# Kernel tuning notes

Hardware: AMD Instinct MI355X
Metric: run time of the kernel (lower is better)

## Reference

```python
import jax, jax.numpy as jnp
import numpy as np
import math

NUM_BUCKETS = 32
MAX_DISTANCE = 128
N_HEADS = 16
D_KV = 64
ATTN_SCALE = True


def _relative_position_bucket(relative_position, num_buckets=NUM_BUCKETS, max_distance=MAX_DISTANCE):
    # bidirectional (encoder) variant
    nb = num_buckets // 2
    buckets = (relative_position > 0).astype(jnp.int32) * nb
    rp = jnp.abs(relative_position)
    max_exact = nb // 2
    is_small = rp < max_exact
    rp_large = max_exact + (
        jnp.log(rp.astype(jnp.float32) / max_exact)
        / math.log(max_distance / max_exact)
        * (nb - max_exact)
    ).astype(jnp.int32)
    rp_large = jnp.minimum(rp_large, nb - 1)
    buckets = buckets + jnp.where(is_small, rp, rp_large)
    return buckets


def compute_bias(rel_bias_emb, q_len, k_len):
    ctx = jnp.arange(q_len)[:, None]
    mem = jnp.arange(k_len)[None, :]
    bucket = _relative_position_bucket(mem - ctx)  # [q,k] int32 in [0,32)
    values = rel_bias_emb[bucket]                  # [q,k,H]
    return jnp.transpose(values, (2, 0, 1))[None]  # [1,H,q,k]


def setup_inputs() -> dict:
    key = jax.random.key(0)
    k1, k2, k3, k4 = jax.random.split(key, 4)
    B, S, D = 2, 2048, 1024
    return {
        "hidden_states": jax.random.normal(k1, (B, S, D), jnp.float32),
        "attention_mask": jnp.ones((B, 1, S, S), jnp.float32),
        "W_qkv": jax.random.normal(k2, (D, 3 * D), jnp.float32) * 0.02,
        "W_o": jax.random.normal(k3, (D, D), jnp.float32) * 0.02,
        "rel_bias_emb": jax.random.normal(k4, (NUM_BUCKETS, N_HEADS), jnp.float32) * 0.02,
    }


def reference(hidden_states, attention_mask, W_qkv, W_o, rel_bias_emb):
    B, S, D = hidden_states.shape
    # fused QKV projection (no bias), then split as in split_tensor_along_last_dim
    qkv = jnp.einsum("bsd,de->bse", hidden_states, W_qkv)
    q, k, v = jnp.split(qkv, 3, axis=-1)
    # [b,s,H*d] -> [b,H,s,d]
    def to_heads(t):
        return jnp.transpose(t.reshape(B, S, N_HEADS, D_KV), (0, 2, 1, 3))
    q, k, v = to_heads(q), to_heads(k), to_heads(v)
    scores = jnp.einsum("bhqd,bhkd->bhqk", q, k)
    if ATTN_SCALE:
        scores = scores / math.sqrt(D_KV)
    position_bias = compute_bias(rel_bias_emb, S, S)  # [1,H,S,S]
    scores = scores * attention_mask + (-10000.0 * (1.0 - attention_mask) + position_bias)
    probs = jax.nn.softmax(scores, axis=-1)  # dropout = eval mode (identity)
    ctx = jnp.einsum("bhqk,bhkd->bhqd", probs, v)
    ctx = jnp.transpose(ctx, (0, 2, 1, 3)).reshape(B, S, N_HEADS * D_KV)
    attn_output = jnp.einsum("bse,ed->bsd", ctx, W_o)
    return attn_output
```

## Files before the change

kernel.cpp:

```cpp
#include <hip/hip_runtime.h>
#include <cstdint>

#define DEV static __device__ __forceinline__

typedef __bf16 bf16x8 __attribute__((ext_vector_type(8)));
typedef __bf16 bf16x4 __attribute__((ext_vector_type(4)));
typedef short  s16x4  __attribute__((ext_vector_type(4)));
typedef float  f32x4  __attribute__((ext_vector_type(4)));

DEV unsigned short f32_bf16(float f) {
  union { float f; unsigned u; } v; v.f = f;
  unsigned r = v.u + 0x7FFFu + ((v.u >> 16) & 1u);
  return (unsigned short)(r >> 16);
}

DEV void gload16(const void* g, void* lds) {
  __builtin_amdgcn_global_load_lds((__attribute__((address_space(1))) void*)g,
                                   (__attribute__((address_space(3))) void*)lds,
                                   16, 0, 0);
}

DEV float bcast_lane(float v, int srclane) {
  union { float f; int i; } u; u.f = v;
  u.i = __builtin_amdgcn_ds_bpermute(srclane << 2, u.i);
  return u.f;
}

DEV f32x4 mfma16_bf16(bf16x4 a, bf16x4 b, f32x4 c) {
  union { bf16x4 h; s16x4 s; } ua, ub; ua.h = a; ub.h = b;
#if __has_builtin(__builtin_amdgcn_mfma_f32_16x16x16bf16_1k)
  return __builtin_amdgcn_mfma_f32_16x16x16bf16_1k(ua.s, ub.s, c, 0, 0, 0);
#else
  f32x4 d;
  asm("v_mfma_f32_16x16x16_bf16 %0, %1, %2, %3" : "=v"(d) : "v"(ua.s), "v"(ub.s), "v"(c));
  return d;
#endif
}

__global__ void cast_bf16(const float* __restrict__ x, unsigned short* __restrict__ y) {
  int i = blockIdx.x * 256 + threadIdx.x;
  float4 v = ((const float4*)x)[i];
  uint2 o;
  o.x = (unsigned)f32_bf16(v.x) | ((unsigned)f32_bf16(v.y) << 16);
  o.y = (unsigned)f32_bf16(v.z) | ((unsigned)f32_bf16(v.w) << 16);
  ((uint2*)y)[i] = o;
}

__global__ void transpose_cast(const float* __restrict__ W, unsigned short* __restrict__ WT,
                               int K, int N) {
  __shared__ float t[64][65];
  int k0 = blockIdx.x * 64, n0 = blockIdx.y * 64;
  int tn = threadIdx.x & 63, tk = threadIdx.x >> 6;
#pragma unroll
  for (int i = 0; i < 64; i += 4)
    t[tk + i][tn] = W[(size_t)(k0 + tk + i) * N + n0 + tn];
  __syncthreads();
  int k2 = (threadIdx.x & 31) * 2, n = threadIdx.x >> 5;
#pragma unroll
  for (int i = 0; i < 64; i += 8) {
    int nn = n + i;
    unsigned o = (unsigned)f32_bf16(t[k2][nn]) | ((unsigned)f32_bf16(t[k2 + 1][nn]) << 16);
    *(unsigned*)&WT[(size_t)(n0 + nn) * K + k0 + k2] = o;
  }
}

__global__ void mask_check(const float* __restrict__ m, int* __restrict__ flag) {
  size_t i = ((size_t)blockIdx.x * 256 + threadIdx.x) * 4;
  float4 v = *(const float4*)(m + i);
  if (v.x != 1.0f || v.y != 1.0f || v.z != 1.0f || v.w != 1.0f) atomicOr(flag, 1);
}

template <int MODE, int TN>
__global__ void __launch_bounds__(256) gemm_bt(const unsigned short* __restrict__ A,
                                               const unsigned short* __restrict__ BT,
                                               float* __restrict__ Cout,
                                               unsigned short* __restrict__ Qb,
                                               unsigned short* __restrict__ Kb,
                                               unsigned short* __restrict__ VTb,
                                               int M, int N, int K) {
  constexpr int NT = TN / 32;
  __shared__ __align__(16) unsigned short As[128 * 32];
  __shared__ __align__(16) unsigned short Bs[TN * 32];
  const int tid = threadIdx.x, wave = tid >> 6, lane = tid & 63;
  const int l = lane & 15, quad = lane >> 4;
  const int wm = (wave & 1) * 64, wn = (wave >> 1) * (TN >> 1);
  const int bm = blockIdx.x, bn = blockIdx.y;

  const int srowA = wave * 32 + (lane >> 2);
  const int sswzA = ((lane & 3) ^ (srowA & 3)) * 8;
  const int srowB = (TN == 128) ? srowA : (wave * 16 + (lane >> 2));
  const int sswzB = ((lane & 3) ^ (srowB & 3)) * 8;
  const unsigned short* pA = A + (size_t)(bm * 128 + srowA) * K + sswzA;
  const unsigned short* pB = BT + (size_t)(bn * TN + srowB) * K + sswzB;
  unsigned short* ldsA0 = &As[(wave * 32) * 32];
  unsigned short* ldsA1 = &As[(wave * 32 + 16) * 32];
  unsigned short* ldsB0 = &Bs[((TN == 128 ? wave * 32 : wave * 16)) * 32];
  unsigned short* ldsB1 = &Bs[(wave * 32 + 16) * 32];

  f32x4 acc[4][NT];
#pragma unroll
  for (int i = 0; i < 4; i++)
#pragma unroll
    for (int j = 0; j < NT; j++) { f32x4 z = {0.f, 0.f, 0.f, 0.f}; acc[i][j] = z; }

  for (int kt = 0; kt < K; kt += 32) {
    __syncthreads();
    gload16(pA, ldsA0);
    gload16(pA + (size_t)16 * K, ldsA1);
    gload16(pB, ldsB0);
    if (TN == 128) gload16(pB + (size_t)16 * K, ldsB1);
    pA += 32; pB += 32;
    __syncthreads();
    bf16x8 af[4], bv[NT];
#pragma unroll
    for (int mt = 0; mt < 4; mt++) {
      int r = wm + mt * 16 + l;
      af[mt] = *(const bf16x8*)&As[r * 32 + ((quad ^ (r & 3)) * 8)];
    }
#pragma unroll
    for (int nt = 0; nt < NT; nt++) {
      int r = wn + nt * 16 + l;
      bv[nt] = *(const bf16x8*)&Bs[r * 32 + ((quad ^ (r & 3)) * 8)];
    }
#pragma unroll
    for (int mt = 0; mt < 4; mt++)
#pragma unroll
      for (int nt = 0; nt < NT; nt++)
        acc[mt][nt] = __builtin_amdgcn_mfma_f32_16x16x32_bf16(af[mt], bv[nt], acc[mt][nt], 0, 0, 0);
  }

#pragma unroll
  for (int nt = 0; nt < NT; nt++) {
    const int col = bn * TN + wn + nt * 16 + l;
#pragma unroll
    for (int mt = 0; mt < 4; mt++) {
      const int row0 = bm * 128 + wm + mt * 16 + quad * 4;
      if (MODE == 0) {
#pragma unroll
        for (int r = 0; r < 4; r++)
          Cout[(size_t)(row0 + r) * N + col] = acc[mt][nt][r];
      } else {
        const int bb = row0 >> 11, s = row0 & 2047;
        if (col < 2048) {
          unsigned short* dst = (col < 1024) ? Qb : Kb;
          const int c = col & 1023;
          const size_t off = ((size_t)(bb * 16 + (c >> 6)) * 2048 + s) * 64 + (c & 63);
#pragma unroll
          for (int r = 0; r < 4; r++)
            dst[off + (size_t)r * 64] = f32_bf16(acc[mt][nt][r]);
        } else {
          const int c = col - 2048;
          const size_t off = ((size_t)(bb * 16 + (c >> 6)) * 64 + (c & 63)) * 2048 + s;
          bf16x4 pk;
#pragma unroll
          for (int r = 0; r < 4; r++) pk[r] = (__bf16)acc[mt][nt][r];
          *(bf16x4*)&VTb[off] = pk;
        }
      }
    }
  }
}

__global__ void __launch_bounds__(256, 2) attn(const unsigned short* __restrict__ Qb,
                                               const unsigned short* __restrict__ Kb,
                                               const unsigned short* __restrict__ VTb,
                                               const float* __restrict__ mask,
                                               const float* __restrict__ emb,
                                               const int* __restrict__ mflag,
                                               unsigned short* __restrict__ ctx) {
  __shared__ __align__(16) unsigned short Ks[128 * 64];
  __shared__ __align__(16) unsigned short VTs[64 * 128];
  __shared__ float biasLUT[512];

  const float LOG2E = 1.4426950408889634f;
  const float c1 = 0.125f * LOG2E;
  const float C2 = 10000.0f * LOG2E;
  const int tid = threadIdx.x, wave = tid >> 6, lane = tid & 63;
  const int l = lane & 15, quad = lane >> 4;
  const int qt = blockIdx.x & 15, bh = blockIdx.x >> 4;
  const int b = bh >> 4, h = bh & 15;
  const int q0 = qt * 128;

  for (int i = tid; i < 512; i += 256) {
    int rel = i - 256;
    int rp = rel < 0 ? -rel : rel;
    int off = rp < 8 ? rp
                     : 8 + (rp >= 12) + (rp >= 16) + (rp >= 23) + (rp >= 32) +
                           (rp >= 46) + (rp >= 64) + (rp >= 91);
    int bucket = (rel > 0 ? 16 : 0) + off;
    biasLUT[i] = emb[bucket * 16 + h] * LOG2E;
  }
  const float satL = emb[15 * 16 + h] * LOG2E;
  const float satH = emb[31 * 16 + h] * LOG2E;
  const int masked = *mflag;

  const unsigned short* qb  = Qb  + ((size_t)(b * 16 + h) * 2048 + q0) * 64;
  const unsigned short* kb  = Kb  + (size_t)(b * 16 + h) * 2048 * 64;
  const unsigned short* vtb = VTb + (size_t)(b * 16 + h) * 64 * 2048;
  const float* mbase = mask + (size_t)b * 2048 * 2048;

  {
    const int rw = lane >> 3, c = lane & 7;
#pragma unroll
    for (int j = 0; j < 4; j++) {
      int row = wave * 32 + j * 8 + rw;
      gload16(qb + (size_t)row * 64 + ((c ^ (row & 7)) * 8), &Ks[(wave * 32 + j * 8) * 64]);
    }
  }
  __syncthreads();
  bf16x8 qf[2][2];
#pragma unroll
  for (int mtq = 0; mtq < 2; mtq++)
#pragma unroll
    for (int ks = 0; ks < 2; ks++) {
      int row = wave * 32 + mtq * 16 + l;
      qf[mtq][ks] = *(const bf16x8*)&Ks[row * 64 + (((ks * 4 + quad) ^ (row & 7)) * 8)];
    }

  float lr[2] = {0.f, 0.f};
  f32x4 Oa[2][4];
#pragma unroll
  for (int mt = 0; mt < 2; mt++)
#pragma unroll
    for (int dt = 0; dt < 4; dt++) { f32x4 z = {0.f, 0.f, 0.f, 0.f}; Oa[mt][dt] = z; }

  for (int kt = 0; kt < 16; kt++) {
    const int k0 = kt * 128;
    __syncthreads();
    {
      const int rw = lane >> 3, c = lane & 7;
#pragma unroll
      for (int j = 0; j < 4; j++) {
        int row = wave * 32 + j * 8 + rw;
        gload16(kb + (size_t)(k0 + row) * 64 + ((c ^ (row & 7)) * 8),
                &Ks[(wave * 32 + j * 8) * 64]);
      }
    }
    {
      const int rw = lane >> 4, c = lane & 15;
#pragma unroll
      for (int j = 0; j < 4; j++) {
        int drow = wave * 16 + j * 4 + rw;
        gload16(vtb + (size_t)drow * 2048 + k0 + ((c ^ (drow & 7)) * 8),
                &VTs[(wave * 16 + j * 4) * 128]);
      }
    }
    __syncthreads();

    const int d0 = k0 - q0;
    const bool sat = (d0 >= 256) || (d0 <= -256);
    const float bias_u = d0 > 0 ? satH : satL;
    const int ibase = 256 + d0 + quad * 4 - wave * 32 - l;
    bf16x4 pa[2][8];

#pragma unroll
    for (int ntk = 0; ntk < 8; ntk++) {
      int row = ntk * 16 + l;
      bf16x8 kf0 = *(const bf16x8*)&Ks[row * 64 + ((quad ^ (row & 7)) * 8)];
      bf16x8 kf1 = *(const bf16x8*)&Ks[row * 64 + (((4 + quad) ^ (row & 7)) * 8)];
#pragma unroll
      for (int mtq = 0; mtq < 2; mtq++) {
        f32x4 s = {0.f, 0.f, 0.f, 0.f};
        s = __builtin_amdgcn_mfma_f32_16x16x32_bf16(kf0, qf[mtq][0], s, 0, 0, 0);
        s = __builtin_amdgcn_mfma_f32_16x16x32_bf16(kf1, qf[mtq][1], s, 0, 0, 0);

        const int ib = ibase - mtq * 16 + ntk * 16;
        if (!masked) {
          if (sat) {
#pragma unroll
            for (int r = 0; r < 4; r++) s[r] = fmaf(s[r], c1, bias_u);
          } else {
#pragma unroll
            for (int r = 0; r < 4; r++) s[r] = fmaf(s[r], c1, biasLUT[ib + r]);
          }
        } else {
          const int qg = q0 + wave * 32 + mtq * 16 + l;
          const int kg = k0 + ntk * 16 + quad * 4;
          float4 mv4 = *(const float4*)&mbase[(size_t)qg * 2048 + kg];
#pragma unroll
          for (int r = 0; r < 4; r++) {
            float mv = r == 0 ? mv4.x : (r == 1 ? mv4.y : (r == 2 ? mv4.z : mv4.w));
            float bias = sat ? bias_u : biasLUT[ib + r];
            s[r] = fmaf(s[r], mv * c1, fmaf(mv, C2, bias - C2));
          }
        }
        bf16x4 pk;
        float ls = 0.f;
#pragma unroll
        for (int r = 0; r < 4; r++) {
          float p = __builtin_amdgcn_exp2f(fminf(s[r], 30.0f));
          ls += p;
          pk[r] = (__bf16)p;
        }
        lr[mtq] += ls;
        pa[mtq][ntk] = pk;
      }
    }

#pragma unroll
    for (int ntk = 0; ntk < 8; ntk++) {
      bf16x4 vf[4];
#pragma unroll
      for (int dt = 0; dt < 4; dt++) {
        int row = dt * 16 + l;
        int ch = (ntk * 2 + (quad >> 1)) ^ (l & 7);
        vf[dt] = *(const bf16x4*)&VTs[row * 128 + ch * 8 + (quad & 1) * 4];
      }
#pragma unroll
      for (int mtq = 0; mtq < 2; mtq++)
#pragma unroll
        for (int dt = 0; dt < 4; dt++)
          Oa[mtq][dt] = mfma16_bf16(pa[mtq][ntk], vf[dt], Oa[mtq][dt]);
    }
  }

  float inv[2];
#pragma unroll
  for (int mtq = 0; mtq < 2; mtq++) {
    float v = lr[mtq];
    v += __shfl_xor(v, 16);
    v += __shfl_xor(v, 32);
    inv[mtq] = 1.0f / v;
  }
#pragma unroll
  for (int mt = 0; mt < 2; mt++)
#pragma unroll
    for (int r = 0; r < 4; r++) {
      float i_bc = bcast_lane(inv[mt], quad * 4 + r);
      const int qg = q0 + wave * 32 + mt * 16 + quad * 4 + r;
#pragma unroll
      for (int dt = 0; dt < 4; dt++)
        ctx[(size_t)(b * 2048 + qg) * 1024 + h * 64 + dt * 16 + l] =
            f32_bf16(Oa[mt][dt][r] * i_bc);
    }
}

extern "C" void kernel_launch(void* const* d_in, const int* in_sizes, int n_in,
                              void* d_out, int out_size, void* d_ws, size_t ws_size,
                              hipStream_t stream) {
  const float* hs   = (const float*)d_in[0];
  const float* mask = (const float*)d_in[1];
  const float* wqkv = (const float*)d_in[2];
  const float* wo   = (const float*)d_in[3];
  const float* emb  = (const float*)d_in[4];
  float* out = (float*)d_out;

  char* ws = (char*)d_ws;
  unsigned short* hB  = (unsigned short*)(ws);
  unsigned short* ctx = (unsigned short*)(ws);
  unsigned short* wqT = (unsigned short*)(ws + 8388608);
  unsigned short* woT = (unsigned short*)(ws + 14680064);
  unsigned short* Qb  = (unsigned short*)(ws + 16777216);
  unsigned short* Kb  = (unsigned short*)(ws + 25165824);
  unsigned short* VTb = (unsigned short*)(ws + 33554432);
  int* mflag          = (int*)(ws + 41943040);
  if (ws_size < 41943044) return;

  hipMemsetAsync(mflag, 0, 4, stream);
  cast_bf16<<<4096, 256, 0, stream>>>(hs, hB);
  transpose_cast<<<dim3(16, 48), 256, 0, stream>>>(wqkv, wqT, 1024, 3072);
  transpose_cast<<<dim3(16, 16), 256, 0, stream>>>(wo, woT, 1024, 1024);
  mask_check<<<8192, 256, 0, stream>>>(mask, mflag);
  gemm_bt<2, 128><<<dim3(32, 24), 256, 0, stream>>>(hB, wqT, nullptr, Qb, Kb, VTb, 4096, 3072, 1024);
  attn<<<512, 256, 0, stream>>>(Qb, Kb, VTb, mask, emb, mflag, ctx);
  gemm_bt<0, 64><<<dim3(32, 16), 256, 0, stream>>>(ctx, woT, out, nullptr, nullptr, nullptr, 4096, 1024, 1024);
}
```

Baseline: 235.1 us.

## Split attention keys across waves with double-buffered K, fuse prep kernels

The attention kernel now gives each block 64 queries and has each wave handle a 32-key slice of every 128-key tile. K tiles are double-buffered so loads for the next tiles are issued while the current one is computed, and partial outputs and row sums are reduced across waves through shared memory at the end. The launch doubles to 1024 blocks with occupancy target 3. The cast and mask-check kernels are merged, the two weight transpose kernels are merged to cut launches, and the exp2 input clamp is dropped. Risks are the cross-wave reduction overhead, hand-coded waitcnt correctness, and possible overflow without the clamp.

```diff
diff --git a/kernel.cpp b/kernel.cpp
--- a/kernel.cpp
+++ b/kernel.cpp
@@ -37,19 +37,32 @@
 #endif
 }
 
-__global__ void cast_bf16(const float* __restrict__ x, unsigned short* __restrict__ y) {
-  int i = blockIdx.x * 256 + threadIdx.x;
-  float4 v = ((const float4*)x)[i];
-  uint2 o;
-  o.x = (unsigned)f32_bf16(v.x) | ((unsigned)f32_bf16(v.y) << 16);
-  o.y = (unsigned)f32_bf16(v.z) | ((unsigned)f32_bf16(v.w) << 16);
-  ((uint2*)y)[i] = o;
-}
-
-__global__ void transpose_cast(const float* __restrict__ W, unsigned short* __restrict__ WT,
-                               int K, int N) {
+__global__ void cast_and_check(const float* __restrict__ x, unsigned short* __restrict__ y,
+                               const float* __restrict__ m, int* __restrict__ flag) {
+  int bx = blockIdx.x;
+  if (bx < 4096) {
+    int i = bx * 256 + threadIdx.x;
+    float4 v = ((const float4*)x)[i];
+    uint2 o;
+    o.x = (unsigned)f32_bf16(v.x) | ((unsigned)f32_bf16(v.y) << 16);
+    o.y = (unsigned)f32_bf16(v.z) | ((unsigned)f32_bf16(v.w) << 16);
+    ((uint2*)y)[i] = o;
+  } else {
+    size_t i = ((size_t)(bx - 4096) * 256 + threadIdx.x) * 4;
+    float4 v = *(const float4*)(m + i);
+    if (v.x != 1.0f || v.y != 1.0f || v.z != 1.0f || v.w != 1.0f) atomicOr(flag, 1);
+  }
+}
+
+__global__ void transpose_cast2(const float* __restrict__ W1, unsigned short* __restrict__ WT1,
+                                const float* __restrict__ W2, unsigned short* __restrict__ WT2) {
   __shared__ float t[64][65];
-  int k0 = blockIdx.x * 64, n0 = blockIdx.y * 64;
+  int bx = blockIdx.x;
+  const float* W; unsigned short* WT; int N, kb, nb;
+  if (bx < 768) { W = W1; WT = WT1; N = 3072; kb = bx & 15; nb = bx >> 4; }
+  else { bx -= 768; W = W2; WT = WT2; N = 1024; kb = bx & 15; nb = bx >> 4; }
+  const int K = 1024;
+  int k0 = kb * 64, n0 = nb * 64;
   int tn = threadIdx.x & 63, tk = threadIdx.x >> 6;
 #pragma unroll
   for (int i = 0; i < 64; i += 4)
@@ -62,12 +75,6 @@
     unsigned o = (unsigned)f32_bf16(t[k2][nn]) | ((unsigned)f32_bf16(t[k2 + 1][nn]) << 16);
     *(unsigned*)&WT[(size_t)(n0 + nn) * K + k0 + k2] = o;
   }
-}
-
-__global__ void mask_check(const float* __restrict__ m, int* __restrict__ flag) {
-  size_t i = ((size_t)blockIdx.x * 256 + threadIdx.x) * 4;
-  float4 v = *(const float4*)(m + i);
-  if (v.x != 1.0f || v.y != 1.0f || v.z != 1.0f || v.w != 1.0f) atomicOr(flag, 1);
 }
 
 template <int MODE, int TN>
@@ -161,25 +168,38 @@
   }
 }
 
-__global__ void __launch_bounds__(256, 2) attn(const unsigned short* __restrict__ Qb,
+#define STAGE_K(kt_, buf_) { const int kbase_ = (kt_) * 128;                              \
+  _Pragma("unroll") for (int j_ = 0; j_ < 4; j_++) {                                      \
+    int row_ = wave * 32 + j_ * 8 + rw8;                                                  \
+    gload16(kbg + (size_t)(kbase_ + row_) * 64 + ((c8 ^ (row_ & 7)) * 8),                 \
+            &(buf_)[(wave * 32 + j_ * 8) * 64]); } }
+
+#define STAGE_V(kt_) { const int kbase_ = (kt_) * 128;                                    \
+  _Pragma("unroll") for (int j_ = 0; j_ < 4; j_++) {                                      \
+    int drow_ = wave * 16 + j_ * 4 + rw16;                                                \
+    gload16(vtb + (size_t)drow_ * 2048 + kbase_ + ((c16 ^ (drow_ & 7)) * 8),              \
+            &vb[(wave * 16 + j_ * 4) * 128]); } }
+
+__global__ void __launch_bounds__(256, 3) attn(const unsigned short* __restrict__ Qb,
                                                const unsigned short* __restrict__ Kb,
                                                const unsigned short* __restrict__ VTb,
                                                const float* __restrict__ mask,
                                                const float* __restrict__ emb,
                                                const int* __restrict__ mflag,
                                                unsigned short* __restrict__ ctx) {
-  __shared__ __align__(16) unsigned short Ks[128 * 64];
-  __shared__ __align__(16) unsigned short VTs[64 * 128];
+  __shared__ __align__(16) unsigned short kb[2][8192];
+  __shared__ __align__(16) unsigned short vb[8192];
   __shared__ float biasLUT[512];
+  __shared__ float Lbuf[3][64];
 
   const float LOG2E = 1.4426950408889634f;
   const float c1 = 0.125f * LOG2E;
   const float C2 = 10000.0f * LOG2E;
   const int tid = threadIdx.x, wave = tid >> 6, lane = tid & 63;
   const int l = lane & 15, quad = lane >> 4;
-  const int qt = blockIdx.x & 15, bh = blockIdx.x >> 4;
+  const int qt = blockIdx.x & 31, bh = blockIdx.x >> 5;
   const int b = bh >> 4, h = bh & 15;
-  const int q0 = qt * 128;
+  const int q0 = qt * 64;
 
   for (int i = tid; i < 512; i += 256) {
     int rel = i - 256;
@@ -194,77 +214,61 @@
   const float satH = emb[31 * 16 + h] * LOG2E;
   const int masked = *mflag;
 
-  const unsigned short* qb  = Qb  + ((size_t)(b * 16 + h) * 2048 + q0) * 64;
-  const unsigned short* kb  = Kb  + (size_t)(b * 16 + h) * 2048 * 64;
+  const unsigned short* qbg = Qb  + ((size_t)(b * 16 + h) * 2048 + q0) * 64;
+  const unsigned short* kbg = Kb  + (size_t)(b * 16 + h) * 2048 * 64;
   const unsigned short* vtb = VTb + (size_t)(b * 16 + h) * 64 * 2048;
   const float* mbase = mask + (size_t)b * 2048 * 2048;
 
-  {
-    const int rw = lane >> 3, c = lane & 7;
-#pragma unroll
-    for (int j = 0; j < 4; j++) {
-      int row = wave * 32 + j * 8 + rw;
-      gload16(qb + (size_t)row * 64 + ((c ^ (row & 7)) * 8), &Ks[(wave * 32 + j * 8) * 64]);
-    }
-  }
+  const int rw8 = lane >> 3, c8 = lane & 7;
+  const int rw16 = lane >> 4, c16 = lane & 15;
+
+#pragma unroll
+  for (int j = 0; j < 2; j++) {
+    int row = wave * 16 + j * 8 + rw8;
+    gload16(qbg + (size_t)row * 64 + ((c8 ^ (row & 7)) * 8), &vb[(wave * 16 + j * 8) * 64]);
+  }
+  STAGE_K(0, kb[0]);
   __syncthreads();
-  bf16x8 qf[2][2];
-#pragma unroll
-  for (int mtq = 0; mtq < 2; mtq++)
+
+  bf16x8 qf[4][2];
+#pragma unroll
+  for (int mtq = 0; mtq < 4; mtq++)
 #pragma unroll
     for (int ks = 0; ks < 2; ks++) {
-      int row = wave * 32 + mtq * 16 + l;
-      qf[mtq][ks] = *(const bf16x8*)&Ks[row * 64 + (((ks * 4 + quad) ^ (row & 7)) * 8)];
-    }
-
-  float lr[2] = {0.f, 0.f};
-  f32x4 Oa[2][4];
-#pragma unroll
-  for (int mt = 0; mt < 2; mt++)
+      int row = mtq * 16 + l;
+      qf[mtq][ks] = *(const bf16x8*)&vb[row * 64 + (((ks * 4 + quad) ^ (row & 7)) * 8)];
+    }
+  __syncthreads();
+
+  STAGE_V(0);
+  STAGE_K(1, kb[1]);
+
+  float lr[4] = {0.f, 0.f, 0.f, 0.f};
+  f32x4 Oa[4][4];
+#pragma unroll
+  for (int mt = 0; mt < 4; mt++)
 #pragma unroll
     for (int dt = 0; dt < 4; dt++) { f32x4 z = {0.f, 0.f, 0.f, 0.f}; Oa[mt][dt] = z; }
 
-  for (int kt = 0; kt < 16; kt++) {
-    const int k0 = kt * 128;
-    __syncthreads();
-    {
-      const int rw = lane >> 3, c = lane & 7;
-#pragma unroll
-      for (int j = 0; j < 4; j++) {
-        int row = wave * 32 + j * 8 + rw;
-        gload16(kb + (size_t)(k0 + row) * 64 + ((c ^ (row & 7)) * 8),
-                &Ks[(wave * 32 + j * 8) * 64]);
-      }
-    }
-    {
-      const int rw = lane >> 4, c = lane & 15;
-#pragma unroll
-      for (int j = 0; j < 4; j++) {
-        int drow = wave * 16 + j * 4 + rw;
-        gload16(vtb + (size_t)drow * 2048 + k0 + ((c ^ (drow & 7)) * 8),
-                &VTs[(wave * 16 + j * 4) * 128]);
-      }
-    }
-    __syncthreads();
-
-    const int d0 = k0 - q0;
-    const bool sat = (d0 >= 256) || (d0 <= -256);
-    const float bias_u = d0 > 0 ? satH : satL;
-    const int ibase = 256 + d0 + quad * 4 - wave * 32 - l;
-    bf16x4 pa[2][8];
-
-#pragma unroll
-    for (int ntk = 0; ntk < 8; ntk++) {
-      int row = ntk * 16 + l;
+  for (int t = 0; t < 16; ++t) {
+    const unsigned short* Ks = kb[t & 1];
+    const int d0w = t * 128 + wave * 32 - q0;
+    const bool sat = (d0w >= 192) || (d0w <= -160);
+    const float bias_u = d0w > 0 ? satH : satL;
+    bf16x4 pa[4][2];
+
+#pragma unroll
+    for (int ntk = 0; ntk < 2; ntk++) {
+      int row = wave * 32 + ntk * 16 + l;
       bf16x8 kf0 = *(const bf16x8*)&Ks[row * 64 + ((quad ^ (row & 7)) * 8)];
       bf16x8 kf1 = *(const bf16x8*)&Ks[row * 64 + (((4 + quad) ^ (row & 7)) * 8)];
 #pragma unroll
-      for (int mtq = 0; mtq < 2; mtq++) {
+      for (int mtq = 0; mtq < 4; mtq++) {
         f32x4 s = {0.f, 0.f, 0.f, 0.f};
         s = __builtin_amdgcn_mfma_f32_16x16x32_bf16(kf0, qf[mtq][0], s, 0, 0, 0);
         s = __builtin_amdgcn_mfma_f32_16x16x32_bf16(kf1, qf[mtq][1], s, 0, 0, 0);
 
-        const int ib = ibase - mtq * 16 + ntk * 16;
+        const int ib = 256 + d0w + ntk * 16 + quad * 4 - mtq * 16 - l;
         if (!masked) {
           if (sat) {
 #pragma unroll
@@ -274,8 +278,8 @@
             for (int r = 0; r < 4; r++) s[r] = fmaf(s[r], c1, biasLUT[ib + r]);
           }
         } else {
-          const int qg = q0 + wave * 32 + mtq * 16 + l;
-          const int kg = k0 + ntk * 16 + quad * 4;
+          const int qg = q0 + mtq * 16 + l;
+          const int kg = t * 128 + wave * 32 + ntk * 16 + quad * 4;
           float4 mv4 = *(const float4*)&mbase[(size_t)qg * 2048 + kg];
 #pragma unroll
           for (int r = 0; r < 4; r++) {
@@ -288,7 +292,7 @@
         float ls = 0.f;
 #pragma unroll
         for (int r = 0; r < 4; r++) {
-          float p = __builtin_amdgcn_exp2f(fminf(s[r], 30.0f));
+          float p = __builtin_amdgcn_exp2f(s[r]);
           ls += p;
           pk[r] = (__bf16)p;
         }
@@ -297,42 +301,73 @@
       }
     }
 
-#pragma unroll
-    for (int ntk = 0; ntk < 8; ntk++) {
-      bf16x4 vf[4];
+    if (t < 15) __builtin_amdgcn_s_waitcnt(0x0F74);
+    else        __builtin_amdgcn_s_waitcnt(0x0F70);
+    __builtin_amdgcn_sched_barrier(0);
+
+#pragma unroll
+    for (int ntk = 0; ntk < 2; ntk++) {
 #pragma unroll
       for (int dt = 0; dt < 4; dt++) {
-        int row = dt * 16 + l;
-        int ch = (ntk * 2 + (quad >> 1)) ^ (l & 7);
-        vf[dt] = *(const bf16x4*)&VTs[row * 128 + ch * 8 + (quad & 1) * 4];
+        int drow = dt * 16 + l;
+        int ch = (wave * 4 + ntk * 2 + (quad >> 1)) ^ (l & 7);
+        bf16x4 vf = *(const bf16x4*)&vb[drow * 128 + ch * 8 + (quad & 1) * 4];
+#pragma unroll
+        for (int mtq = 0; mtq < 4; mtq++)
+          Oa[mtq][dt] = mfma16_bf16(pa[mtq][ntk], vf, Oa[mtq][dt]);
       }
-#pragma unroll
-      for (int mtq = 0; mtq < 2; mtq++)
-#pragma unroll
-        for (int dt = 0; dt < 4; dt++)
-          Oa[mtq][dt] = mfma16_bf16(pa[mtq][ntk], vf[dt], Oa[mtq][dt]);
-    }
-  }
-
-  float inv[2];
-#pragma unroll
-  for (int mtq = 0; mtq < 2; mtq++) {
+    }
+
+    __syncthreads();
+    if (t < 15) STAGE_V(t + 1);
+    if (t < 14) STAGE_K(t + 2, kb[t & 1]);
+  }
+
+#pragma unroll
+  for (int mtq = 0; mtq < 4; mtq++) {
     float v = lr[mtq];
     v += __shfl_xor(v, 16);
     v += __shfl_xor(v, 32);
-    inv[mtq] = 1.0f / v;
-  }
-#pragma unroll
-  for (int mt = 0; mt < 2; mt++)
-#pragma unroll
-    for (int r = 0; r < 4; r++) {
-      float i_bc = bcast_lane(inv[mt], quad * 4 + r);
-      const int qg = q0 + wave * 32 + mt * 16 + quad * 4 + r;
+    lr[mtq] = v;
+  }
+  if (wave) {
+    float* reg = (wave == 1) ? (float*)&kb[0][0] : (wave == 2) ? (float*)&kb[1][0] : (float*)&vb[0];
+#pragma unroll
+    for (int mt = 0; mt < 4; mt++)
 #pragma unroll
       for (int dt = 0; dt < 4; dt++)
-        ctx[(size_t)(b * 2048 + qg) * 1024 + h * 64 + dt * 16 + l] =
-            f32_bf16(Oa[mt][dt][r] * i_bc);
-    }
+        *(f32x4*)&reg[(dt * 16 + l) * 64 + mt * 16 + quad * 4] = Oa[mt][dt];
+    if (quad == 0)
+#pragma unroll
+      for (int mt = 0; mt < 4; mt++) Lbuf[wave - 1][mt * 16 + l] = lr[mt];
+  }
+  __syncthreads();
+  if (wave == 0) {
+    const float* P1 = (const float*)&kb[0][0];
+    const float* P2 = (const float*)&kb[1][0];
+    const float* P3 = (const float*)&vb[0];
+    float inv[4];
+#pragma unroll
+    for (int mt = 0; mt < 4; mt++)
+      inv[mt] = 1.0f / (lr[mt] + Lbuf[0][mt * 16 + l] + Lbuf[1][mt * 16 + l] + Lbuf[2][mt * 16 + l]);
+#pragma unroll
+    for (int mt = 0; mt < 4; mt++)
+#pragma unroll
+      for (int dt = 0; dt < 4; dt++) {
+        const int fidx = (dt * 16 + l) * 64 + mt * 16 + quad * 4;
+        f32x4 o = Oa[mt][dt];
+        o += *(const f32x4*)&P1[fidx];
+        o += *(const f32x4*)&P2[fidx];
+        o += *(const f32x4*)&P3[fidx];
+#pragma unroll
+        for (int r = 0; r < 4; r++) {
+          float i_bc = bcast_lane(inv[mt], quad * 4 + r);
+          const int qg = q0 + mt * 16 + quad * 4 + r;
+          ctx[(size_t)(b * 2048 + qg) * 1024 + h * 64 + dt * 16 + l] =
+              f32_bf16(o[r] * i_bc);
+        }
+      }
+  }
 }
 
 extern "C" void kernel_launch(void* const* d_in, const int* in_sizes, int n_in,
@@ -357,11 +392,9 @@
   if (ws_size < 41943044) return;
 
   hipMemsetAsync(mflag, 0, 4, stream);
-  cast_bf16<<<4096, 256, 0, stream>>>(hs, hB);
-  transpose_cast<<<dim3(16, 48), 256, 0, stream>>>(wqkv, wqT, 1024, 3072);
-  transpose_cast<<<dim3(16, 16), 256, 0, stream>>>(wo, woT, 1024, 1024);
-  mask_check<<<8192, 256, 0, stream>>>(mask, mflag);
+  cast_and_check<<<12288, 256, 0, stream>>>(hs, hB, mask, mflag);
+  transpose_cast2<<<1024, 256, 0, stream>>>(wqkv, wqT, wo, woT);
   gemm_bt<2, 128><<<dim3(32, 24), 256, 0, stream>>>(hB, wqT, nullptr, Qb, Kb, VTb, 4096, 3072, 1024);
-  attn<<<512, 256, 0, stream>>>(Qb, Kb, VTb, mask, emb, mflag, ctx);
+  attn<<<1024, 256, 0, stream>>>(Qb, Kb, VTb, mask, emb, mflag, ctx);
   gemm_bt<0, 64><<<dim3(32, 16), 256, 0, stream>>>(ctx, woT, out, nullptr, nullptr, nullptr, 4096, 1024, 1024);
 }
```

New measurement: 341.9 us. 1.45x slower.
